# Kernel tuning notes

Hardware: AMD Instinct MI355X
Metric: run time of the kernel (lower is better)

Reference implementation:

```python
import jax, jax.numpy as jnp
import numpy as np

KH, KW = 4, 4
N, P, IN_CH, OUT_CH = 50000, 32, 64, 64


def setup_inputs() -> dict:
    key = jax.random.key(0)
    k1, k2, k3, k4 = jax.random.split(key, 4)
    features = jax.random.normal(k1, (N, IN_CH), jnp.float32)
    receivers = jax.random.randint(k2, (N, P), 0, N)
    # relative offsets scaled so most neighbors fall inside the support radius
    relative_positions = jax.random.normal(k3, (N, P, 2), jnp.float32) * 0.35
    window_support = jnp.float32(1.0)
    a = 3  # window exponent (1 - d^2/R^2)^a
    kernel = jax.random.uniform(k4, (KH, KW, IN_CH, OUT_CH), jnp.float32, -0.05, 0.05)
    bias = jnp.zeros((OUT_CH,), jnp.float32)
    return {"features": features, "receivers": receivers,
            "relative_positions": relative_positions,
            "window_support": window_support, "a": a,
            "kernel": kernel, "bias": bias}


def reference(features, receivers, relative_positions, window_support, a, kernel, bias):
    kh, kw, in_ch, out_ch = kernel.shape
    n, p = receivers.shape
    g_bins = kh * kw

    gathered = features[receivers]                      # [N,P,in] gather
    r = relative_positions / window_support             # normalized to [-1,1]
    d2 = jnp.sum(r * r, axis=-1)                        # [N,P]
    win = jnp.maximum(1.0 - d2, 0.0) ** a               # radial window

    # map normalized position to continuous kernel-grid coordinates
    gy = jnp.clip((r[..., 0] + 1.0) * 0.5 * (kh - 1), 0.0, kh - 1)
    gx = jnp.clip((r[..., 1] + 1.0) * 0.5 * (kw - 1), 0.0, kw - 1)
    y0 = jnp.clip(jnp.floor(gy).astype(jnp.int32), 0, kh - 2)
    x0 = jnp.clip(jnp.floor(gx).astype(jnp.int32), 0, kw - 2)
    fy = gy - y0
    fx = gx - x0

    # accumulate window*bilinear-weighted features into kernel bins per output point,
    # avoiding materializing a per-edge [in,out] interpolated filter
    n_idx = jnp.arange(n)[:, None]                      # broadcasts over P
    M = jnp.zeros((n, g_bins, in_ch), features.dtype)
    corners = [(0, 0, (1 - fy) * (1 - fx)), (0, 1, (1 - fy) * fx),
               (1, 0, fy * (1 - fx)), (1, 1, fy * fx)]
    for dy, dx, bw in corners:
        g = (y0 + dy) * kw + (x0 + dx)                  # [N,P] flat bin index
        M = M.at[n_idx, g].add((bw * win)[..., None] * gathered)

    out = jnp.einsum('ngi,gio->no', M, kernel.reshape(g_bins, in_ch, out_ch))
    return out / p + bias
```

## Files before the change

### kernel.cpp

```cpp
#include <hip/hip_runtime.h>
#include <hip/hip_bf16.h>

typedef unsigned short u16;
typedef unsigned int u32;

#define THREADS 256
constexpr int CH = 64;
constexpr int PP = 32;
constexpr int TM = 16;

constexpr int W_OFF  = 0;
constexpr int MB_OFF = 16384;
constexpr int LDS_BYTES = 49152;

typedef __attribute__((ext_vector_type(8))) short short8;
typedef __attribute__((ext_vector_type(4))) float f32x4;

static __device__ __forceinline__ u16 f2bf_rne(float f) {
  __hip_bfloat16 h = __float2bfloat16(f);
  return __builtin_bit_cast(u16, h);
}
static __device__ __forceinline__ u16 rbf(float f) {
  u32 u = __builtin_bit_cast(u32, f);
  return (u16)((u + 0x8000u) >> 16);
}

__global__ void prep_feat(const float* __restrict__ in, u16* __restrict__ outb, int n2) {
  int i = blockIdx.x * blockDim.x + threadIdx.x;
  if (i < n2) {
    float2 v = ((const float2*)in)[i];
    u32 u = (u32)f2bf_rne(v.x) | ((u32)f2bf_rne(v.y) << 16);
    ((u32*)outb)[i] = u;
  }
}

__global__ void prep_k2f(const float* __restrict__ kern, u16* __restrict__ k2f) {
  int d = blockIdx.x * blockDim.x + threadIdx.x;
  int e = d & 7, l = (d >> 3) & 63, ot = (d >> 9) & 3, ks = d >> 11;
  int k = ks * 32 + (l >> 4) * 8 + e;
  int o = ot * 16 + (l & 15);
  k2f[d] = f2bf_rne(kern[k * 64 + o]);
}

#define LOADQ(qv, A4_, B4_) do {                                                \
    u32 vo[8];                                                                  \
    vo[0] = (u32)(A4_).x * 64u + (u32)l15; vo[1] = (u32)(A4_).y * 64u + (u32)l15; \
    vo[2] = (u32)(A4_).z * 64u + (u32)l15; vo[3] = (u32)(A4_).w * 64u + (u32)l15; \
    vo[4] = (u32)(B4_).x * 64u + (u32)l15; vo[5] = (u32)(B4_).y * 64u + (u32)l15; \
    vo[6] = (u32)(B4_).z * 64u + (u32)l15; vo[7] = (u32)(B4_).w * 64u + (u32)l15; \
    _Pragma("unroll")                                                           \
    for (int ib = 0; ib < 4; ++ib)                                              \
      _Pragma("unroll")                                                         \
      for (int e = 0; e < 8; ++e) qv[ib * 8 + e] = (u32)fbf[vo[e] + ib * 16];   \
  } while (0)

#define COMPUTE(t_, qv) do {                                                    \
    const int m_c = wid * 4 + (t_);                                             \
    const short8 af = *(const short8*)(smem + W_OFF + m_c * 1024 + l15 * 64 + l4 * 16); \
    f32x4 accm[4];                                                              \
    _Pragma("unroll")                                                           \
    for (int ib = 0; ib < 4; ++ib) {                                            \
      union { u32 u[4]; short8 s; } bb;                                         \
      _Pragma("unroll")                                                         \
      for (int j = 0; j < 4; ++j)                                               \
        bb.u[j] = qv[ib * 8 + 2 * j] | (qv[ib * 8 + 2 * j + 1] << 16);          \
      const f32x4 cz = {0.f, 0.f, 0.f, 0.f};                                    \
      accm[ib] = __builtin_amdgcn_mfma_f32_16x16x32_bf16(af, bb.s, cz, 0, 0, 0);\
    }                                                                           \
    _Pragma("unroll")                                                           \
    for (int ib = 0; ib < 4; ++ib)                                              \
      _Pragma("unroll")                                                         \
      for (int r = 0; r < 4; ++r) {                                             \
        const int g = l4 * 4 + r;                                               \
        const u32 k = (u32)(g * 64 + ib * 16 + l15);                            \
        u32 byt = (u32)m_c * 2048u + k * 2u;                                    \
        byt ^= ((u32)((m_c & 7) ^ (g & 7)) << 4);                               \
        *(u16*)(smem + MB_OFF + byt) = rbf(accm[ib][r]);                        \
      }                                                                         \
  } while (0)

__global__ __launch_bounds__(THREADS, 3) void cconv_main(
    const int* __restrict__ recv, const float* __restrict__ relpos,
    const float* __restrict__ wsup, const int* __restrict__ aptr,
    const u16* __restrict__ fbf, const u16* __restrict__ k2f,
    const float* __restrict__ bias, float* __restrict__ out) {
  __shared__ __align__(16) char smem[LDS_BYTES];
  const int tid = threadIdx.x;
  const int n0 = blockIdx.x * TM;
  const int wid = tid >> 6, lane = tid & 63;
  const int l15 = lane & 15, l4 = lane >> 4;

  const int* rbase = recv + (n0 + wid * 4) * PP + l4 * 8;
  const int4 A40 = *(const int4*)(rbase + 0 * PP);
  const int4 B40 = *(const int4*)(rbase + 0 * PP + 4);
  const int4 A41 = *(const int4*)(rbase + 1 * PP);
  const int4 B41 = *(const int4*)(rbase + 1 * PP + 4);
  const int4 A42 = *(const int4*)(rbase + 2 * PP);
  const int4 B42 = *(const int4*)(rbase + 2 * PP + 4);
  const int4 A43 = *(const int4*)(rbase + 3 * PP);
  const int4 B43 = *(const int4*)(rbase + 3 * PP + 4);

  {
    const float invws = 1.0f / wsup[0];
    int a = aptr[0];
    if (a < 0 || a > 64) a = (int)(*(const float*)aptr);
    #pragma unroll
    for (int ee = 0; ee < 2; ++ee) {
      const int e = tid + ee * 256;
      const int m = e >> 5, p = e & 31;
      const int ei = (n0 + m) * PP + p;
      const float2 rp2 = ((const float2*)relpos)[ei];
      const float rx = rp2.x * invws, ry = rp2.y * invws;
      const float d2 = rx * rx + ry * ry;
      const float w1 = fmaxf(1.0f - d2, 0.0f);
      float win = 1.0f;
      for (int q = 0; q < a; ++q) win *= w1;
      float gy = fminf(fmaxf((rx + 1.0f) * 1.5f, 0.0f), 3.0f);
      float gx = fminf(fmaxf((ry + 1.0f) * 1.5f, 0.0f), 3.0f);
      int y0 = (int)gy; y0 = y0 > 2 ? 2 : y0;
      int x0 = (int)gx; x0 = x0 > 2 ? 2 : x0;
      const float fy = gy - (float)y0, fx = gx - (float)x0;
      u16* wp = (u16*)(smem + W_OFF) + m * 512 + p;
      #pragma unroll
      for (int g = 0; g < 16; ++g) {
        const int y = g >> 2, x = g & 3;
        const float wyv = (y == y0) ? (1.0f - fy) : (y == y0 + 1) ? fy : 0.0f;
        const float wxv = (x == x0) ? (1.0f - fx) : (x == x0 + 1) ? fx : 0.0f;
        wp[g * 32] = rbf(win * wyv * wxv);
      }
    }
  }
  __syncthreads();

  {
    u32 q0[32], q1[32], q2[32], q3[32];
    LOADQ(q0, A40, B40);
    LOADQ(q1, A41, B41);
    COMPUTE(0, q0);
    LOADQ(q2, A42, B42);
    COMPUTE(1, q1);
    LOADQ(q3, A43, B43);
    COMPUTE(2, q2);
    COMPUTE(3, q3);
  }
  __syncthreads();

  f32x4 acc = {0.f, 0.f, 0.f, 0.f};
  {
    const u32 rowb = (u32)l15 * 2048u;
    const u32 swl = (u32)(l15 & 7) << 4;
    #pragma unroll 8
    for (int ks = 0; ks < 32; ++ks) {
      const u32 kc = (u32)ks * 32u + (u32)l4 * 8u;
      const u32 g7 = (((kc >> 6) & 7u) << 4);
      const u32 byt = (rowb + kc * 2u) ^ swl ^ g7;
      const short8 a2 = *(const short8*)(smem + MB_OFF + byt);
      const short8 b2 = *(const short8*)(k2f + ((u32)(ks * 4 + wid) * 64u + (u32)lane) * 8u);
      acc = __builtin_amdgcn_mfma_f32_16x16x32_bf16(a2, b2, acc, 0, 0, 0);
    }
  }

  const int o = wid * 16 + l15;
  const float bv = bias[o];
  #pragma unroll
  for (int r = 0; r < 4; ++r)
    out[(n0 + l4 * 4 + r) * CH + o] = acc[r] * (1.0f / 32.0f) + bv;
}

extern "C" void kernel_launch(void* const* d_in, const int* in_sizes, int n_in,
                              void* d_out, int out_size, void* d_ws, size_t ws_size,
                              hipStream_t stream) {
  const float* features = (const float*)d_in[0];
  const int* receivers  = (const int*)d_in[1];
  const float* relpos   = (const float*)d_in[2];
  const float* wsup     = (const float*)d_in[3];
  const int* aptr       = (const int*)d_in[4];
  const float* kern     = (const float*)d_in[5];
  const float* bias     = (const float*)d_in[6];
  float* out = (float*)d_out;

  const int N = in_sizes[0] / CH;
  u16* fbf = (u16*)d_ws;
  u16* k2f = (u16*)((char*)d_ws + (size_t)N * CH * 2);

  const int nfeat2 = in_sizes[0] / 2;
  prep_feat<<<dim3((nfeat2 + 255) / 256), dim3(256), 0, stream>>>(features, fbf, nfeat2);
  prep_k2f<<<dim3(65536 / 256), dim3(256), 0, stream>>>(kern, k2f);

  cconv_main<<<dim3(N / TM), dim3(THREADS), 0, stream>>>(
      receivers, relpos, wsup, aptr, fbf, k2f, bias, out);
}
```

Before: 54.95 us.

## Stage gathered feature rows into LDS via async global_load_lds double buffering

Replaces scalar 2-byte global gathers of bf16 feature rows with 16-byte global_load_lds transfers into a per-wave double-buffered LDS region, then reads operands from LDS for the MFMA. Loads for later rows are issued while earlier rows are being computed, with explicit vmcnt waits. LDS grows to 80KB via dynamic shared memory and launch bounds drop to 2 blocks per CU, trading occupancy for wider, asynchronous memory traffic.

```diff
diff --git a/kernel.cpp b/kernel.cpp
--- a/kernel.cpp
+++ b/kernel.cpp
@@ -3,6 +3,7 @@
 
 typedef unsigned short u16;
 typedef unsigned int u32;
+typedef unsigned long long u64;
 
 #define THREADS 256
 constexpr int CH = 64;
@@ -11,7 +12,8 @@
 
 constexpr int W_OFF  = 0;
 constexpr int MB_OFF = 16384;
-constexpr int LDS_BYTES = 49152;
+constexpr int F_OFF  = 49152;
+constexpr int LDS_BYTES = 81920;
 
 typedef __attribute__((ext_vector_type(8))) short short8;
 typedef __attribute__((ext_vector_type(4))) float f32x4;
@@ -42,28 +44,38 @@
   k2f[d] = f2bf_rne(kern[k * 64 + o]);
 }
 
-#define LOADQ(qv, A4_, B4_) do {                                                \
-    u32 vo[8];                                                                  \
-    vo[0] = (u32)(A4_).x * 64u + (u32)l15; vo[1] = (u32)(A4_).y * 64u + (u32)l15; \
-    vo[2] = (u32)(A4_).z * 64u + (u32)l15; vo[3] = (u32)(A4_).w * 64u + (u32)l15; \
-    vo[4] = (u32)(B4_).x * 64u + (u32)l15; vo[5] = (u32)(B4_).y * 64u + (u32)l15; \
-    vo[6] = (u32)(B4_).z * 64u + (u32)l15; vo[7] = (u32)(B4_).w * 64u + (u32)l15; \
-    _Pragma("unroll")                                                           \
-    for (int ib = 0; ib < 4; ++ib)                                              \
-      _Pragma("unroll")                                                         \
-      for (int e = 0; e < 8; ++e) qv[ib * 8 + e] = (u32)fbf[vo[e] + ib * 16];   \
+#define GLL0(g_, l_) __builtin_amdgcn_global_load_lds(                          \
+    (const __attribute__((address_space(1))) unsigned int*)(const void*)(g_),   \
+    (__attribute__((address_space(3))) unsigned int*)(void*)(l_), 16, 0, 0)
+
+#define ISSUE(rv_, buf_) do {                                                   \
+    __builtin_amdgcn_sched_barrier(0);                                          \
+    const char* s_ = fb + (size_t)(u32)(rv_) * 128u + h16;                      \
+    char* d_ = Fw + (buf_) * 4096;                                              \
+    u64 sa0 = (u64)(s_ + 0);  asm("" : "+v"(sa0));                              \
+    u64 sa1 = (u64)(s_ + 32); asm("" : "+v"(sa1));                              \
+    u64 sa2 = (u64)(s_ + 64); asm("" : "+v"(sa2));                              \
+    u64 sa3 = (u64)(s_ + 96); asm("" : "+v"(sa3));                              \
+    GLL0(sa0, d_ + 0);                                                          \
+    GLL0(sa1, d_ + 1024);                                                       \
+    GLL0(sa2, d_ + 2048);                                                       \
+    GLL0(sa3, d_ + 3072);                                                       \
   } while (0)
 
-#define COMPUTE(t_, qv) do {                                                    \
-    const int m_c = wid * 4 + (t_);                                             \
-    const short8 af = *(const short8*)(smem + W_OFF + m_c * 1024 + l15 * 64 + l4 * 16); \
+#define BUILDP(t_, buf_) do {                                                   \
+    const int m_b = wid * 4 + (t_);                                             \
+    const char* Fb = Fw + (buf_) * 4096;                                        \
+    const short8 af = *(const short8*)(smem + W_OFF + m_b * 1024 + l15 * 64 + l4 * 16); \
     f32x4 accm[4];                                                              \
     _Pragma("unroll")                                                           \
     for (int ib = 0; ib < 4; ++ib) {                                            \
+      u32 q[8];                                                                 \
+      _Pragma("unroll")                                                         \
+      for (int e = 0; e < 8; ++e)                                               \
+        q[e] = (u32)*(const u16*)(Fb + ib * 1024 + (e * 4 + l4) * 32 + l15 * 2);\
       union { u32 u[4]; short8 s; } bb;                                         \
       _Pragma("unroll")                                                         \
-      for (int j = 0; j < 4; ++j)                                               \
-        bb.u[j] = qv[ib * 8 + 2 * j] | (qv[ib * 8 + 2 * j + 1] << 16);          \
+      for (int j = 0; j < 4; ++j) bb.u[j] = q[2 * j] | (q[2 * j + 1] << 16);    \
       const f32x4 cz = {0.f, 0.f, 0.f, 0.f};                                    \
       accm[ib] = __builtin_amdgcn_mfma_f32_16x16x32_bf16(af, bb.s, cz, 0, 0, 0);\
     }                                                                           \
@@ -73,32 +85,35 @@
       for (int r = 0; r < 4; ++r) {                                             \
         const int g = l4 * 4 + r;                                               \
         const u32 k = (u32)(g * 64 + ib * 16 + l15);                            \
-        u32 byt = (u32)m_c * 2048u + k * 2u;                                    \
-        byt ^= ((u32)((m_c & 7) ^ (g & 7)) << 4);                               \
+        u32 byt = (u32)m_b * 2048u + k * 2u;                                    \
+        byt ^= ((u32)((m_b & 7) ^ (g & 7)) << 4);                               \
         *(u16*)(smem + MB_OFF + byt) = rbf(accm[ib][r]);                        \
       }                                                                         \
   } while (0)
 
-__global__ __launch_bounds__(THREADS, 3) void cconv_main(
+__global__ __launch_bounds__(THREADS, 2) void cconv_main(
     const int* __restrict__ recv, const float* __restrict__ relpos,
     const float* __restrict__ wsup, const int* __restrict__ aptr,
     const u16* __restrict__ fbf, const u16* __restrict__ k2f,
     const float* __restrict__ bias, float* __restrict__ out) {
-  __shared__ __align__(16) char smem[LDS_BYTES];
+  extern __shared__ __align__(16) char smem[];
   const int tid = threadIdx.x;
   const int n0 = blockIdx.x * TM;
   const int wid = tid >> 6, lane = tid & 63;
   const int l15 = lane & 15, l4 = lane >> 4;
 
-  const int* rbase = recv + (n0 + wid * 4) * PP + l4 * 8;
-  const int4 A40 = *(const int4*)(rbase + 0 * PP);
-  const int4 B40 = *(const int4*)(rbase + 0 * PP + 4);
-  const int4 A41 = *(const int4*)(rbase + 1 * PP);
-  const int4 B41 = *(const int4*)(rbase + 1 * PP + 4);
-  const int4 A42 = *(const int4*)(rbase + 2 * PP);
-  const int4 B42 = *(const int4*)(rbase + 2 * PP + 4);
-  const int4 A43 = *(const int4*)(rbase + 3 * PP);
-  const int4 B43 = *(const int4*)(rbase + 3 * PP + 4);
+  char* Fw = smem + F_OFF + wid * 8192;
+  const char* fb = (const char*)fbf;
+  const int h16 = (lane & 1) * 16;
+
+  const int rho = lane >> 1;
+  const int e_l = ((rho & 3) << 3) | (rho >> 2);
+  const int* rq = recv + (n0 + wid * 4) * PP + e_l;
+  int rv0 = rq[0], rv1 = rq[PP], rv2 = rq[2 * PP], rv3 = rq[3 * PP];
+  asm volatile("" : "+v"(rv0), "+v"(rv1), "+v"(rv2), "+v"(rv3));
+
+  ISSUE(rv0, 0);
+  ISSUE(rv1, 1);
 
   {
     const float invws = 1.0f / wsup[0];
@@ -132,17 +147,14 @@
   }
   __syncthreads();
 
-  {
-    u32 q0[32], q1[32], q2[32], q3[32];
-    LOADQ(q0, A40, B40);
-    LOADQ(q1, A41, B41);
-    COMPUTE(0, q0);
-    LOADQ(q2, A42, B42);
-    COMPUTE(1, q1);
-    LOADQ(q3, A43, B43);
-    COMPUTE(2, q2);
-    COMPUTE(3, q3);
-  }
+  BUILDP(0, 0);
+  ISSUE(rv2, 0);
+  BUILDP(1, 1);
+  ISSUE(rv3, 1);
+  asm volatile("s_waitcnt vmcnt(4)" ::: "memory");
+  BUILDP(2, 0);
+  asm volatile("s_waitcnt vmcnt(0)" ::: "memory");
+  BUILDP(3, 1);
   __syncthreads();
 
   f32x4 acc = {0.f, 0.f, 0.f, 0.f};
@@ -187,6 +199,8 @@
   prep_feat<<<dim3((nfeat2 + 255) / 256), dim3(256), 0, stream>>>(features, fbf, nfeat2);
   prep_k2f<<<dim3(65536 / 256), dim3(256), 0, stream>>>(kern, k2f);
 
-  cconv_main<<<dim3(N / TM), dim3(THREADS), 0, stream>>>(
+  hipFuncSetAttribute((const void*)cconv_main,
+                      hipFuncAttributeMaxDynamicSharedMemorySize, LDS_BYTES);
+  cconv_main<<<dim3(N / TM), dim3(THREADS), LDS_BYTES, stream>>>(
       receivers, relpos, wsup, aptr, fbf, k2f, bias, out);
 }
```

Result: slower. 62.67 us (+14.1%).
